# Optimization experiments

Measured on AMD Instinct MI355X. Metric: run time of the kernel, lower is better.

## Reference

```python
import jax, jax.numpy as jnp
import numpy as np

NUM_GRAPHS = 64
NUM_EDGE_TYPES = 3


def gat_conv(x, src, dst, W, a_src, a_dst, bias, num_nodes, heads, ch):
    # PyG GATConv, concat=False: mean over heads, attention leaky_relu slope 0.2
    xp = (x @ W).reshape(num_nodes, heads, ch)          # [N,H,C]
    al_s = jnp.einsum('nhc,hc->nh', xp, a_src)           # [N,H]
    al_d = jnp.einsum('nhc,hc->nh', xp, a_dst)
    logits = jax.nn.leaky_relu(al_s[src] + al_d[dst], 0.2)  # [E,H]
    m = jax.ops.segment_max(logits, dst, num_segments=num_nodes)
    e = jnp.exp(logits - m[dst])
    denom = jax.ops.segment_sum(e, dst, num_segments=num_nodes)
    alpha = e / denom[dst]                               # segment softmax over dst
    msg = alpha[:, :, None] * xp[src]                    # [E,H,C]
    out = jax.ops.segment_sum(msg, dst, num_segments=num_nodes)  # [N,H,C]
    return out.mean(axis=1) + bias


def lstm_dir(seq, w_ih, w_hh, b_ih, b_hh):
    # seq: [L,N,C]; PyTorch LSTM cell math
    hh = w_hh.shape[1]
    n = seq.shape[1]
    def step(carry, xt):
        h, c = carry
        g = xt @ w_ih.T + b_ih + h @ w_hh.T + b_hh
        i, f, gg, o = jnp.split(g, 4, axis=-1)
        c = jax.nn.sigmoid(f) * c + jax.nn.sigmoid(i) * jnp.tanh(gg)
        h = jax.nn.sigmoid(o) * jnp.tanh(c)
        return (h, c), h
    init = (jnp.zeros((n, hh), seq.dtype), jnp.zeros((n, hh), seq.dtype))
    _, hs = jax.lax.scan(step, init, seq)
    return hs  # [L,N,hh]


def setup_inputs() -> dict:
    key = jax.random.key(0)
    ks = jax.random.split(key, 24)
    N, E, C, H, P, T = 50000, 600000, 128, 4, 2, NUM_EDGE_TYPES
    HH = (P * C) // 2  # JK biLSTM hidden = 128
    s = 0.05
    src = jax.random.randint(ks[0], (E,), 0, N, dtype=jnp.int32)
    off = jax.random.randint(ks[1], (E,), 1, N, dtype=jnp.int32)
    dst = (src + off) % N  # guaranteed self-loop free
    edge_index = jnp.stack([src, dst], axis=0)  # types are contiguous blocks of E//T
    batch = jnp.sort(jax.random.randint(ks[2], (N,), 0, NUM_GRAPHS, dtype=jnp.int32))
    return {
        'x': jax.random.normal(ks[3], (N, C), jnp.float32),
        'edge_index': edge_index,
        'batch': batch,
        'problem_type': jax.random.uniform(ks[4], (NUM_GRAPHS, 1), jnp.float32),
        'gat_W': jax.random.normal(ks[5], (P, T, C, H * C), jnp.float32) * s,
        'gat_att_src': jax.random.normal(ks[6], (P, T, H, C), jnp.float32) * s,
        'gat_att_dst': jax.random.normal(ks[7], (P, T, H, C), jnp.float32) * s,
        'gat_bias': jnp.zeros((P, T, C), jnp.float32),
        'w_ih_fw': jax.random.normal(ks[8], (4 * HH, C), jnp.float32) * s,
        'w_hh_fw': jax.random.normal(ks[9], (4 * HH, HH), jnp.float32) * s,
        'b_ih_fw': jnp.zeros((4 * HH,), jnp.float32),
        'b_hh_fw': jnp.zeros((4 * HH,), jnp.float32),
        'w_ih_bw': jax.random.normal(ks[10], (4 * HH, C), jnp.float32) * s,
        'w_hh_bw': jax.random.normal(ks[11], (4 * HH, HH), jnp.float32) * s,
        'b_ih_bw': jnp.zeros((4 * HH,), jnp.float32),
        'b_hh_bw': jnp.zeros((4 * HH,), jnp.float32),
        'jk_att_w': jax.random.normal(ks[12], (2 * HH, 1), jnp.float32) * s,
        'jk_att_b': jnp.zeros((1,), jnp.float32),
        'fc1_w': jax.random.normal(ks[13], (C + 1, 80), jnp.float32) * s,
        'fc1_b': jnp.zeros((80,), jnp.float32),
        'fc2_w': jax.random.normal(ks[14], (80, 80), jnp.float32) * s,
        'fc2_b': jnp.zeros((80,), jnp.float32),
        'fc3_w': jax.random.normal(ks[15], (80, 10), jnp.float32) * s,
        'fc3_b': jnp.zeros((10,), jnp.float32),
    }


def reference(x, edge_index, batch, problem_type, gat_W, gat_att_src, gat_att_dst,
              gat_bias, w_ih_fw, w_hh_fw, b_ih_fw, b_hh_fw, w_ih_bw, w_hh_bw,
              b_ih_bw, b_hh_bw, jk_att_w, jk_att_b, fc1_w, fc1_b, fc2_w, fc2_b,
              fc3_w, fc3_b):
    N, C = x.shape
    P, T, H, _ = gat_att_src.shape
    E = edge_index.shape[1]
    Et = E // T  # edge types stored in contiguous blocks
    loop = jnp.arange(N, dtype=edge_index.dtype)
    xs = [x]
    cur = x
    for p in range(P):
        acc = jnp.zeros_like(cur)
        for t in range(T):
            src = jnp.concatenate([edge_index[0, t * Et:(t + 1) * Et], loop])
            dst = jnp.concatenate([edge_index[1, t * Et:(t + 1) * Et], loop])
            out = gat_conv(cur, src, dst, gat_W[p, t], gat_att_src[p, t],
                           gat_att_dst[p, t], gat_bias[p, t], N, H, C)
            acc = acc + jax.nn.leaky_relu(out)  # slope 0.01 (F.leaky_relu default)
        cur = acc / T
        xs.append(cur)
    seq = jnp.stack(xs, axis=0)  # [L,N,C], L=P+1
    hf = lstm_dir(seq, w_ih_fw, w_hh_fw, b_ih_fw, b_hh_fw)
    hb = lstm_dir(seq[::-1], w_ih_bw, w_hh_bw, b_ih_bw, b_hh_bw)[::-1]
    h = jnp.concatenate([hf, hb], axis=-1)  # [L,N,2*HH]
    score = jnp.einsum('lnh,ho->lno', h, jk_att_w)[..., 0] + jk_att_b[0]  # [L,N]
    alpha = jax.nn.softmax(score, axis=0)
    xjk = jnp.einsum('ln,lnc->nc', alpha, seq)  # JK-LSTM weighted sum
    pooled = jax.ops.segment_sum(xjk, batch, num_segments=NUM_GRAPHS)  # collate='sum'
    z = jnp.concatenate([pooled, problem_type], axis=1)
    z = jax.nn.leaky_relu(z @ fc1_w + fc1_b)
    z = jax.nn.leaky_relu(z @ fc2_w + fc2_b)
    return z @ fc3_w + fc3_b
```

## Files before the change

### kernel.cpp

```cpp
#include <hip/hip_runtime.h>
#include <cfloat>


typedef __attribute__((ext_vector_type(8))) short short8;
typedef __attribute__((ext_vector_type(4))) float f32x4;

#define DEG_CAP 32

__device__ __forceinline__ float lrelu(float x, float s) { return x > 0.f ? x : s * x; }

__device__ __forceinline__ float sigmf(float x) {
    return __builtin_amdgcn_rcpf(1.f + __expf(-x));
}
__device__ __forceinline__ float tanhf_fast(float x) {
    x = fminf(fmaxf(x, -15.f), 15.f);
    float e = __expf(2.f * x);
    return (e - 1.f) * __builtin_amdgcn_rcpf(e + 1.f);
}

__device__ __forceinline__ unsigned f2bf(float f) {
    unsigned u = __float_as_uint(f);
    return (u + 0x7FFFu + ((u >> 16) & 1u)) >> 16;
}
__device__ __forceinline__ float bflo(unsigned u) {
    return __uint_as_float(u << 16);
}
__device__ __forceinline__ float bfhi(unsigned u) {
    return __uint_as_float(u & 0xFFFF0000u);
}

__device__ __forceinline__ int xcd_tile(int bid, int nwg) {
    int q = nwg >> 3, r = nwg & 7;
    int xcd = bid & 7, idx = bid >> 3;
    return (xcd < r ? xcd * (q + 1) : r * (q + 1) + (xcd - r) * q) + idx;
}

__device__ __forceinline__ void stage_tiles(
    char* ldsA, char* ldsB, const float* __restrict__ A,
    const ushort* __restrict__ Bt, int row0, int col0, int M, int tid)
{
#pragma unroll
    for (int it = 0; it < 4; ++it) {
        int idx = it * 512 + tid;
        int r = idx >> 4, kc = (idx & 15) << 3;
        int row = row0 + r;
        float4 v0 = make_float4(0.f, 0.f, 0.f, 0.f), v1 = v0;
        if (row < M) {
            const float* ap = A + (long)row * 128 + kc;
            v0 = *(const float4*)ap;
            v1 = *(const float4*)(ap + 4);
        }
        uint4 w;
        w.x = f2bf(v0.x) | (f2bf(v0.y) << 16);
        w.y = f2bf(v0.z) | (f2bf(v0.w) << 16);
        w.z = f2bf(v1.x) | (f2bf(v1.y) << 16);
        w.w = f2bf(v1.z) | (f2bf(v1.w) << 16);
        int off = (r * 256 + kc * 2) ^ ((r & 7) << 4);
        *(uint4*)(ldsA + off) = w;
        *(uint4*)(ldsB + off) = *(const uint4*)(Bt + (long)(col0 + r) * 128 + kc);
    }
}

__device__ __forceinline__ void stage_a16(
    char* ldsA, const ushort* __restrict__ A, int row0, int M, int tid)
{
#pragma unroll
    for (int it = 0; it < 4; ++it) {
        int idx = it * 512 + tid;
        int r = idx >> 4, kc = (idx & 15) << 3;
        int row = row0 + r;
        uint4 v = make_uint4(0, 0, 0, 0);
        if (row < M) v = *(const uint4*)(A + (long)row * 128 + kc);
        *(uint4*)(ldsA + ((r * 256 + kc * 2) ^ ((r & 7) << 4))) = v;
    }
}
__device__ __forceinline__ void stage_b16(
    char* ldsB, const ushort* __restrict__ B, int tid)
{
#pragma unroll
    for (int it = 0; it < 4; ++it) {
        int idx = it * 512 + tid;
        int r = idx >> 4, kc = (idx & 15) << 3;
        *(uint4*)(ldsB + ((r * 256 + kc * 2) ^ ((r & 7) << 4))) =
            *(const uint4*)(B + (long)r * 128 + kc);
    }
}

__device__ __forceinline__ void compute_tile(
    const char* ldsA, const char* ldsB, f32x4 acc[2][4],
    int wr, int wc, int lr, int lk)
{
#pragma unroll
    for (int ks = 0; ks < 4; ++ks) {
        int kb = ks * 64 + lk;
        short8 af[2], bfr[4];
#pragma unroll
        for (int i = 0; i < 2; ++i) {
            int r = wr + i * 16 + lr;
            af[i] = *(const short8*)(ldsA + ((r * 256 + kb) ^ ((r & 7) << 4)));
        }
#pragma unroll
        for (int j = 0; j < 4; ++j) {
            int c = wc + j * 16 + lr;
            bfr[j] = *(const short8*)(ldsB + ((c * 256 + kb) ^ ((c & 7) << 4)));
        }
#pragma unroll
        for (int i = 0; i < 2; ++i)
#pragma unroll
            for (int j = 0; j < 4; ++j)
                acc[i][j] = __builtin_amdgcn_mfma_f32_16x16x32_bf16(af[i], bfr[j], acc[i][j], 0, 0, 0);
    }
}

__global__ __launch_bounds__(512, 4) void gemm_att(
    const float* __restrict__ A, const ushort* __restrict__ Bt,
    ushort* __restrict__ C16, const float* __restrict__ a_s,
    const float* __restrict__ a_d, float* __restrict__ als,
    float* __restrict__ ald, int M, int nwg)
{
    __shared__ char lds[65536];
    __shared__ float smS[128], smD[128];
    char* ldsA = lds;
    char* ldsB = lds + 32768;
    const int tid = threadIdx.x;
    int tile = xcd_tile(blockIdx.x, nwg);
    int row0 = (tile >> 2) * 128;
    int h = tile & 3;
    int col0 = h * 128;
    if (tid < 128) { smS[tid] = 0.f; smD[tid] = 0.f; }
    stage_tiles(ldsA, ldsB, A, Bt, row0, col0, M, tid);
    __syncthreads();

    const int wv = tid >> 6, lane = tid & 63;
    const int wr = (wv & 3) * 32, wc = (wv >> 2) * 64;
    const int lr = lane & 15;
    const int lk = (lane >> 4) << 4;
    f32x4 acc[2][4] = {};
    compute_tile(ldsA, ldsB, acc, wr, wc, lr, lk);

    const float* asl = a_s + h * 128;
    const float* adl = a_d + h * 128;
#pragma unroll
    for (int i = 0; i < 2; ++i) {
#pragma unroll
        for (int q = 0; q < 4; ++q) {
            float ps = 0.f, pd = 0.f;
            int row = row0 + wr + i * 16 + (lane >> 4) * 4 + q;
#pragma unroll
            for (int j = 0; j < 4; ++j) {
                int cc = wc + j * 16 + lr;
                float v = acc[i][j][q];
                ps += v * asl[cc];
                pd += v * adl[cc];
                if (row < M) C16[(long)row * 512 + col0 + cc] = (ushort)f2bf(v);
            }
#pragma unroll
            for (int off = 8; off; off >>= 1) {
                ps += __shfl_xor(ps, off);
                pd += __shfl_xor(pd, off);
            }
            if (lr == 0) {
                int rl = wr + i * 16 + (lane >> 4) * 4 + q;
                atomicAdd(&smS[rl], ps);
                atomicAdd(&smD[rl], pd);
            }
        }
    }
    __syncthreads();
    if (tid < 128) {
        int row = row0 + tid;
        if (row < M) {
            als[(long)row * 4 + h] = smS[tid];
            ald[(long)row * 4 + h] = smD[tid];
        }
    }
}

__global__ __launch_bounds__(512, 4) void lstm_step(
    const ushort* __restrict__ Ab, const ushort* __restrict__ Bih,
    const ushort* __restrict__ Bhh, const ushort* __restrict__ hprev,
    ushort* __restrict__ hcur, float* __restrict__ cbuf,
    const float* __restrict__ bi, const float* __restrict__ bh,
    const float* __restrict__ jw, float* __restrict__ score,
    int N, int nwg, int first)
{
    __shared__ char lds[65536];
    __shared__ float ssc[128];
    char* ldsA = lds;
    char* ldsB = lds + 32768;
    const int tid = threadIdx.x;
    int tile = xcd_tile(blockIdx.x, nwg);
    int row0 = (tile >> 2) * 128;
    int cc = tile & 3;
    if (tid < 128) ssc[tid] = 0.f;

    const int wv = tid >> 6, lane = tid & 63;
    const int wr = (wv & 3) * 32, wc = (wv >> 2) * 64;
    const int lr = lane & 15, lg = lane >> 4;
    const int lk = lg << 4;
    f32x4 acc[2][4] = {};

    stage_a16(ldsA, Ab, row0, N, tid);
    stage_b16(ldsB, Bih + (long)cc * 128 * 128, tid);
    __syncthreads();
    compute_tile(ldsA, ldsB, acc, wr, wc, lr, lk);
    if (!first) {
        __syncthreads();
        stage_a16(ldsA, hprev, row0, N, tid);
        stage_b16(ldsB, Bhh + (long)cc * 128 * 128, tid);
        __syncthreads();
        compute_tile(ldsA, ldsB, acc, wr, wc, lr, lk);
    }

    const int ch = cc * 32 + (wc >> 6) * 16 + lr;
    const float bI = bi[ch] + bh[ch];
    const float bF = bi[128 + ch] + bh[128 + ch];
    const float bG = bi[256 + ch] + bh[256 + ch];
    const float bO = bi[384 + ch] + bh[384 + ch];
    const float jv = jw[ch];
    float psum[8];
#pragma unroll
    for (int i = 0; i < 2; ++i) {
#pragma unroll
        for (int q = 0; q < 4; ++q) {
            int u = i * 4 + q;
            int row = row0 + wr + i * 16 + lg * 4 + q;
            float p = 0.f;
            if (row < N) {
                long off = (long)row * 128 + ch;
                float cprev = first ? 0.f : cbuf[off];
                float cv = sigmf(acc[i][1][q] + bF) * cprev
                         + sigmf(acc[i][0][q] + bI) * tanhf_fast(acc[i][2][q] + bG);
                float hv = sigmf(acc[i][3][q] + bO) * tanhf_fast(cv);
                cbuf[off] = cv;
                hcur[off] = (ushort)f2bf(hv);
                p = hv * jv;
            }
            psum[u] = p;
        }
    }
#pragma unroll
    for (int u = 0; u < 8; ++u) {
        float p = psum[u];
#pragma unroll
        for (int off = 8; off; off >>= 1) p += __shfl_xor(p, off);
        if (lr == 0)
            atomicAdd(&ssc[wr + (u >> 2) * 16 + lg * 4 + (u & 3)], p);
    }
    __syncthreads();
    if (tid < 128) {
        int row = row0 + tid;
        if (row < N) unsafeAtomicAdd(&score[row], ssc[tid]);
    }
}

__global__ void pack_gatw(const float* __restrict__ gw, ushort* __restrict__ out) {
    int i = blockIdx.x * 256 + threadIdx.x;
    if (i >= 6 * 65536) return;
    int pt = i >> 16, rem = i & 65535, n = rem >> 7, k = rem & 127;
    out[i] = (ushort)f2bf(gw[pt * 65536 + k * 512 + n]);
}
__global__ void pack_lstm(const float* __restrict__ a, const float* __restrict__ b,
                          const float* __restrict__ c, const float* __restrict__ d,
                          ushort* __restrict__ out) {
    int i = blockIdx.x * 256 + threadIdx.x;
    if (i >= 4 * 65536) return;
    const float* p = (i < 65536) ? a : (i < 131072) ? b : (i < 196608) ? c : d;
    int rem = i & 65535;
    int cp = rem >> 7, k = rem & 127;
    int g = (cp >> 4) & 3;
    int ch = ((cp >> 6) << 4) | (cp & 15);
    out[i] = (ushort)f2bf(p[(g * 128 + ch) * 128 + k]);
}
__global__ void pack_x(const float* __restrict__ x, ushort* __restrict__ o, long n) {
    long i = ((long)blockIdx.x * 256 + threadIdx.x) * 4;
    if (i >= n) return;
    float4 v = *(const float4*)(x + i);
    ushort4 u;
    u.x = (ushort)f2bf(v.x); u.y = (ushort)f2bf(v.y);
    u.z = (ushort)f2bf(v.z); u.w = (ushort)f2bf(v.w);
    *(ushort4*)(o + i) = u;
}

__global__ __launch_bounds__(256) void build_csr(
    const int* __restrict__ srcs, const int* __restrict__ dsts,
    int E, int Et, int N, int* __restrict__ cnt, int* __restrict__ bucket)
{
    int i = blockIdx.x * 256 + threadIdx.x;
    if (i >= E) return;
    int t = i / Et;
    int s = srcs[i];
    int d = dsts[i];
    int slot = atomicAdd(&cnt[t * N + d], 1);
    if (slot < DEG_CAP) bucket[((long)(t * N + d)) * DEG_CAP + slot] = s;
}

__global__ __launch_bounds__(256) void gat_gather(
    const int* __restrict__ cnt, const int* __restrict__ bucket,
    const float* __restrict__ als, const float* __restrict__ ald,
    const ushort* __restrict__ xp16, const float* __restrict__ bias,
    float* __restrict__ dstb, ushort* __restrict__ out16, int N, int t, int first)
{
    int d = blockIdx.x * 4 + (threadIdx.x >> 6);
    int lane = threadIdx.x & 63;
    if (d >= N) return;
    int deg = min(cnt[t * N + d], DEG_CAP);
    int s = d;
    if (lane < deg) s = bucket[((long)(t * N + d)) * DEG_CAP + lane];
    bool act = (lane <= deg);
    float4 ad = *(const float4*)(ald + (long)d * 4);
    float l0 = -FLT_MAX, l1 = -FLT_MAX, l2 = -FLT_MAX, l3 = -FLT_MAX;
    if (act) {
        float4 as = *(const float4*)(als + (long)s * 4);
        l0 = lrelu(as.x + ad.x, 0.2f);
        l1 = lrelu(as.y + ad.y, 0.2f);
        l2 = lrelu(as.z + ad.z, 0.2f);
        l3 = lrelu(as.w + ad.w, 0.2f);
    }
    float m0 = l0, m1 = l1, m2 = l2, m3 = l3;
#pragma unroll
    for (int off = 32; off; off >>= 1) {
        m0 = fmaxf(m0, __shfl_xor(m0, off));
        m1 = fmaxf(m1, __shfl_xor(m1, off));
        m2 = fmaxf(m2, __shfl_xor(m2, off));
        m3 = fmaxf(m3, __shfl_xor(m3, off));
    }
    float e0 = 0.f, e1 = 0.f, e2 = 0.f, e3 = 0.f;
    if (act) {
        e0 = __expf(l0 - m0); e1 = __expf(l1 - m1);
        e2 = __expf(l2 - m2); e3 = __expf(l3 - m3);
    }
    float s0 = e0, s1 = e1, s2 = e2, s3 = e3;
#pragma unroll
    for (int off = 32; off; off >>= 1) {
        s0 += __shfl_xor(s0, off);
        s1 += __shfl_xor(s1, off);
        s2 += __shfl_xor(s2, off);
        s3 += __shfl_xor(s3, off);
    }
    float a0 = 0.25f * e0 / s0, a1 = 0.25f * e1 / s1;
    float a2 = 0.25f * e2 / s2, a3 = 0.25f * e3 / s3;

    float accL = 0.f, accH = 0.f;
    int sj = __shfl(s, 0);
    const uint* xs = (const uint*)(xp16 + (long)sj * 512);
    uint c0 = xs[lane], c1 = xs[64 + lane], c2 = xs[128 + lane], c3 = xs[192 + lane];
    for (int j = 0; j < deg; ++j) {
        int sn = __shfl(s, j + 1);
        const uint* xn = (const uint*)(xp16 + (long)sn * 512);
        uint n0 = xn[lane], n1 = xn[64 + lane], n2 = xn[128 + lane], n3 = xn[192 + lane];
        float w0 = __shfl(a0, j), w1 = __shfl(a1, j);
        float w2 = __shfl(a2, j), w3 = __shfl(a3, j);
        accL += w0 * bflo(c0) + w1 * bflo(c1) + w2 * bflo(c2) + w3 * bflo(c3);
        accH += w0 * bfhi(c0) + w1 * bfhi(c1) + w2 * bfhi(c2) + w3 * bfhi(c3);
        c0 = n0; c1 = n1; c2 = n2; c3 = n3;
    }
    float w0 = __shfl(a0, deg), w1 = __shfl(a1, deg);
    float w2 = __shfl(a2, deg), w3 = __shfl(a3, deg);
    accL += w0 * bflo(c0) + w1 * bflo(c1) + w2 * bflo(c2) + w3 * bflo(c3);
    accH += w0 * bfhi(c0) + w1 * bfhi(c1) + w2 * bfhi(c2) + w3 * bfhi(c3);

    int chL = 2 * lane;
    float r0 = lrelu(accL + bias[chL], 0.01f) * (1.f / 3.f);
    float r1 = lrelu(accH + bias[chL + 1], 0.01f) * (1.f / 3.f);
    float2* ap = (float2*)(dstb + (long)d * 128) + lane;
    float2 f;
    if (first) { f.x = r0; f.y = r1; }
    else       { float2 prev = *ap; f.x = prev.x + r0; f.y = prev.y + r1; }
    *ap = f;
    if (out16) {
        ushort2 u2;
        u2.x = (ushort)f2bf(f.x);
        u2.y = (ushort)f2bf(f.y);
        *((ushort2*)(out16 + (long)d * 128) + lane) = u2;
    }
}

__global__ void jk_kernel(const float* __restrict__ score, const float* __restrict__ x0,
                          const float* __restrict__ x1, const float* __restrict__ x2,
                          float* __restrict__ xjk, int N)
{
    long i = (long)blockIdx.x * 256 + threadIdx.x;
    long n = i >> 7;
    if (n >= N) return;
    float s0 = score[n], s1 = score[N + n], s2 = score[2L * N + n];
    float m = fmaxf(s0, fmaxf(s1, s2));
    float e0 = expf(s0 - m), e1 = expf(s1 - m), e2 = expf(s2 - m);
    float inv = 1.f / (e0 + e1 + e2);
    xjk[i] = (e0 * x0[i] + e1 * x1[i] + e2 * x2[i]) * inv;
}

__global__ void init_z0(const float* __restrict__ ptype, float* __restrict__ z0) {
    int i = blockIdx.x * 128 + threadIdx.x;
    if (i < 64 * 129) z0[i] = ((i % 129) == 128) ? ptype[i / 129] : 0.f;
}

__global__ __launch_bounds__(128) void pool2(
    const float* __restrict__ xjk, const int* __restrict__ batch,
    float* __restrict__ z0, int N)
{
    int c = threadIdx.x;
    int n0 = blockIdx.x * 64;
    if (n0 >= N) return;
    int n1 = min(n0 + 64, N);
    float s = 0.f;
    int g = batch[n0];
    for (int n = n0; n < n1; ++n) {
        int b = batch[n];
        if (b != g) { unsafeAtomicAdd(&z0[g * 129 + c], s); s = 0.f; g = b; }
        s += xjk[(long)n * 128 + c];
    }
    unsafeAtomicAdd(&z0[g * 129 + c], s);
}

__global__ __launch_bounds__(128) void mlp_kernel(
    const float* __restrict__ z0, const float* __restrict__ w1, const float* __restrict__ b1,
    const float* __restrict__ w2, const float* __restrict__ b2,
    const float* __restrict__ w3, const float* __restrict__ b3,
    float* __restrict__ out)
{
    int gidx = blockIdx.x, tid = threadIdx.x;
    __shared__ float zin[129], z1[80], z2[80];
    zin[tid] = z0[gidx * 129 + tid];
    if (tid == 0) zin[128] = z0[gidx * 129 + 128];
    __syncthreads();
    if (tid < 80) {
        float s = b1[tid];
        for (int k = 0; k < 129; ++k) s += zin[k] * w1[k * 80 + tid];
        z1[tid] = lrelu(s, 0.01f);
    }
    __syncthreads();
    if (tid < 80) {
        float s = b2[tid];
        for (int k = 0; k < 80; ++k) s += z1[k] * w2[k * 80 + tid];
        z2[tid] = lrelu(s, 0.01f);
    }
    __syncthreads();
    if (tid < 10) {
        float s = b3[tid];
        for (int k = 0; k < 80; ++k) s += z2[k] * w3[k * 10 + tid];
        out[gidx * 10 + tid] = s;
    }
}

extern "C" void kernel_launch(void* const* d_in, const int* in_sizes, int n_in,
                              void* d_out, int out_size, void* d_ws, size_t ws_size,
                              hipStream_t stream)
{
    (void)n_in; (void)out_size; (void)ws_size;
    const float* x      = (const float*)d_in[0];
    const int*   ei     = (const int*)d_in[1];
    const int*   batch  = (const int*)d_in[2];
    const float* ptype  = (const float*)d_in[3];
    const float* gatW   = (const float*)d_in[4];
    const float* gatAs  = (const float*)d_in[5];
    const float* gatAd  = (const float*)d_in[6];
    const float* gatB   = (const float*)d_in[7];
    const float* w_ih_fw = (const float*)d_in[8];
    const float* w_hh_fw = (const float*)d_in[9];
    const float* b_ih_fw = (const float*)d_in[10];
    const float* b_hh_fw = (const float*)d_in[11];
    const float* w_ih_bw = (const float*)d_in[12];
    const float* w_hh_bw = (const float*)d_in[13];
    const float* b_ih_bw = (const float*)d_in[14];
    const float* b_hh_bw = (const float*)d_in[15];
    const float* jkw    = (const float*)d_in[16];
    const float* fc1w   = (const float*)d_in[18];
    const float* fc1b   = (const float*)d_in[19];
    const float* fc2w   = (const float*)d_in[20];
    const float* fc2b   = (const float*)d_in[21];
    const float* fc3w   = (const float*)d_in[22];
    const float* fc3b   = (const float*)d_in[23];

    const int N = in_sizes[0] / 128;
    const int E = in_sizes[1] / 2;
    const int Et = E / 3;
    const long NC = (long)N * 128;

    float* w = (float*)d_ws;
    float* xp   = w; w += (long)N * 512;
    float* l1   = w; w += NC;
    float* l2   = w; w += NC;
    float* accb = w; w += NC;
    float* outm = w; w += NC;
    ushort* xb16 = (ushort*)w; w += 3L * N * 64;
    float* als  = w; w += (long)N * 4;
    float* ald  = w; w += (long)N * 4;
    float* score = w; w += 3L * N;
    ushort* gwt = (ushort*)w; w += 6 * 65536 / 2;
    ushort* lwt = (ushort*)w; w += 4 * 65536 / 2;
    float* z0   = w; w += 64 * 129 + 4;

    int* cnt    = (int*)outm;
    int* bucket = cnt + 3L * N;
    ushort* xp16 = (ushort*)xp;
    ushort* h0 = xp16 + (long)N * 512;
    ushort* h1 = h0 + NC;

    pack_gatw<<<(6 * 65536 + 255) / 256, 256, 0, stream>>>(gatW, gwt);
    pack_lstm<<<(4 * 65536 + 255) / 256, 256, 0, stream>>>(w_ih_fw, w_hh_fw, w_ih_bw, w_hh_bw, lwt);
    pack_x<<<(int)((NC / 4 + 255) / 256), 256, 0, stream>>>(x, xb16, NC);
    hipMemsetAsync(score, 0, sizeof(float) * 3 * N, stream);
    hipMemsetAsync(cnt, 0, sizeof(int) * 3 * N, stream);
    build_csr<<<(E + 255) / 256, 256, 0, stream>>>(ei, ei + E, E, Et, N, cnt, bucket);

    const int RB = (N + 127) / 128;
    const int nwg = RB * 4;
    const int ncb = (int)((NC + 255) / 256);

    const float* cur = x;
    for (int p = 0; p < 2; ++p) {
        float* dstb = (p == 0) ? l1 : l2;
        ushort* d16 = xb16 + (long)(p + 1) * N * 128;
        for (int t = 0; t < 3; ++t) {
            int pt = p * 3 + t;
            gemm_att<<<nwg, 512, 0, stream>>>(cur, gwt + (long)pt * 65536, xp16,
                                              gatAs + pt * 512, gatAd + pt * 512,
                                              als, ald, N, nwg);
            gat_gather<<<(N + 3) / 4, 256, 0, stream>>>(cnt, bucket, als, ald, xp16,
                                                        gatB + pt * 128, dstb,
                                                        (t == 2) ? d16 : nullptr,
                                                        N, t, t == 0);
        }
        cur = dstb;
    }

    float* cbuf = outm;
    for (int dir = 0; dir < 2; ++dir) {
        const ushort* Bih = lwt + (long)(dir ? 2 : 0) * 65536;
        const ushort* Bhh = lwt + (long)(dir ? 3 : 1) * 65536;
        const float* bi = dir ? b_ih_bw : b_ih_fw;
        const float* bh = dir ? b_hh_bw : b_hh_fw;
        const float* jw = jkw + (dir ? 128 : 0);
        ushort* hp = h0;
        ushort* hc = h1;
        for (int j = 0; j < 3; ++j) {
            int l = dir ? (2 - j) : j;
            const ushort* Ab = xb16 + (long)l * N * 128;
            lstm_step<<<nwg, 512, 0, stream>>>(Ab, Bih, Bhh, hp, hc, cbuf,
                                               bi, bh, jw, score + (long)l * N,
                                               N, nwg, j == 0);
            ushort* tmp = hp; hp = hc; hc = tmp;
        }
    }

    jk_kernel<<<ncb, 256, 0, stream>>>(score, x, l1, l2, accb, N);
    init_z0<<<65, 128, 0, stream>>>(ptype, z0);
    pool2<<<(N + 63) / 64, 128, 0, stream>>>(accb, batch, z0, N);
    mlp_kernel<<<64, 128, 0, stream>>>(z0, fc1w, fc1b, fc2w, fc2b, fc3w, fc3b,
                                       (float*)d_out);
}
```

Baseline: 793.3 us.

## Gather two destinations per wave and feed GEMM pre-packed bf16 activations

The GAT gather kernel now gives each half-wave its own destination node, so each wave covers two nodes. Each lane loads eight packed words per neighbour, and the softmax reductions run over 32 lanes. DEG_CAP drops to 31 so a node's neighbours plus its self loop fit in one half-wave, and the neighbour loop runs to the larger degree of the pair, with zero weights padding the shorter one. Separately, gemm_att now reads the bf16 layer activations that the gather already writes, instead of loading fp32 and converting to bf16 in the kernel. That halves the GEMM's activation read traffic and removes the conversion work.

```diff
diff --git a/kernel.cpp b/kernel.cpp
--- a/kernel.cpp
+++ b/kernel.cpp
@@ -5,7 +5,7 @@
 typedef __attribute__((ext_vector_type(8))) short short8;
 typedef __attribute__((ext_vector_type(4))) float f32x4;
 
-#define DEG_CAP 32
+#define DEG_CAP 31
 
 __device__ __forceinline__ float lrelu(float x, float s) { return x > 0.f ? x : s * x; }
 
@@ -33,32 +33,6 @@
     int q = nwg >> 3, r = nwg & 7;
     int xcd = bid & 7, idx = bid >> 3;
     return (xcd < r ? xcd * (q + 1) : r * (q + 1) + (xcd - r) * q) + idx;
-}
-
-__device__ __forceinline__ void stage_tiles(
-    char* ldsA, char* ldsB, const float* __restrict__ A,
-    const ushort* __restrict__ Bt, int row0, int col0, int M, int tid)
-{
-#pragma unroll
-    for (int it = 0; it < 4; ++it) {
-        int idx = it * 512 + tid;
-        int r = idx >> 4, kc = (idx & 15) << 3;
-        int row = row0 + r;
-        float4 v0 = make_float4(0.f, 0.f, 0.f, 0.f), v1 = v0;
-        if (row < M) {
-            const float* ap = A + (long)row * 128 + kc;
-            v0 = *(const float4*)ap;
-            v1 = *(const float4*)(ap + 4);
-        }
-        uint4 w;
-        w.x = f2bf(v0.x) | (f2bf(v0.y) << 16);
-        w.y = f2bf(v0.z) | (f2bf(v0.w) << 16);
-        w.z = f2bf(v1.x) | (f2bf(v1.y) << 16);
-        w.w = f2bf(v1.z) | (f2bf(v1.w) << 16);
-        int off = (r * 256 + kc * 2) ^ ((r & 7) << 4);
-        *(uint4*)(ldsA + off) = w;
-        *(uint4*)(ldsB + off) = *(const uint4*)(Bt + (long)(col0 + r) * 128 + kc);
-    }
 }
 
 __device__ __forceinline__ void stage_a16(
@@ -113,7 +87,7 @@
 }
 
 __global__ __launch_bounds__(512, 4) void gemm_att(
-    const float* __restrict__ A, const ushort* __restrict__ Bt,
+    const ushort* __restrict__ A16, const ushort* __restrict__ Bt,
     ushort* __restrict__ C16, const float* __restrict__ a_s,
     const float* __restrict__ a_d, float* __restrict__ als,
     float* __restrict__ ald, int M, int nwg)
@@ -128,7 +102,8 @@
     int h = tile & 3;
     int col0 = h * 128;
     if (tid < 128) { smS[tid] = 0.f; smD[tid] = 0.f; }
-    stage_tiles(ldsA, ldsB, A, Bt, row0, col0, M, tid);
+    stage_a16(ldsA, A16, row0, M, tid);
+    stage_b16(ldsB, Bt + (long)col0 * 128, tid);
     __syncthreads();
 
     const int wv = tid >> 6, lane = tid & 63;
@@ -301,13 +276,14 @@
     const ushort* __restrict__ xp16, const float* __restrict__ bias,
     float* __restrict__ dstb, ushort* __restrict__ out16, int N, int t, int first)
 {
-    int d = blockIdx.x * 4 + (threadIdx.x >> 6);
     int lane = threadIdx.x & 63;
-    if (d >= N) return;
+    int half = lane >> 5, hl = lane & 31;
+    int d = blockIdx.x * 8 + (threadIdx.x >> 6) * 2 + half;
+    if (d >= N) d = N - 1;
     int deg = min(cnt[t * N + d], DEG_CAP);
     int s = d;
-    if (lane < deg) s = bucket[((long)(t * N + d)) * DEG_CAP + lane];
-    bool act = (lane <= deg);
+    if (hl < deg) s = bucket[((long)(t * N + d)) * DEG_CAP + hl];
+    bool act = (hl <= deg);
     float4 ad = *(const float4*)(ald + (long)d * 4);
     float l0 = -FLT_MAX, l1 = -FLT_MAX, l2 = -FLT_MAX, l3 = -FLT_MAX;
     if (act) {
@@ -319,7 +295,7 @@
     }
     float m0 = l0, m1 = l1, m2 = l2, m3 = l3;
 #pragma unroll
-    for (int off = 32; off; off >>= 1) {
+    for (int off = 16; off; off >>= 1) {
         m0 = fmaxf(m0, __shfl_xor(m0, off));
         m1 = fmaxf(m1, __shfl_xor(m1, off));
         m2 = fmaxf(m2, __shfl_xor(m2, off));
@@ -332,7 +308,7 @@
     }
     float s0 = e0, s1 = e1, s2 = e2, s3 = e3;
 #pragma unroll
-    for (int off = 32; off; off >>= 1) {
+    for (int off = 16; off; off >>= 1) {
         s0 += __shfl_xor(s0, off);
         s1 += __shfl_xor(s1, off);
         s2 += __shfl_xor(s2, off);
@@ -341,38 +317,62 @@
     float a0 = 0.25f * e0 / s0, a1 = 0.25f * e1 / s1;
     float a2 = 0.25f * e2 / s2, a3 = 0.25f * e3 / s3;
 
-    float accL = 0.f, accH = 0.f;
-    int sj = __shfl(s, 0);
+    int md = deg;
+#pragma unroll
+    for (int off = 32; off; off >>= 1) md = max(md, __shfl_xor(md, off));
+
+    int base = (lane & 32);
+    float accL[4] = {0.f, 0.f, 0.f, 0.f}, accH[4] = {0.f, 0.f, 0.f, 0.f};
+    int sj = __shfl(s, base);
     const uint* xs = (const uint*)(xp16 + (long)sj * 512);
-    uint c0 = xs[lane], c1 = xs[64 + lane], c2 = xs[128 + lane], c3 = xs[192 + lane];
-    for (int j = 0; j < deg; ++j) {
-        int sn = __shfl(s, j + 1);
+    uint c0 = xs[hl], c1 = xs[32 + hl], c2 = xs[64 + hl], c3 = xs[96 + hl];
+    uint c4 = xs[128 + hl], c5 = xs[160 + hl], c6 = xs[192 + hl], c7 = xs[224 + hl];
+    for (int j = 0; j < md; ++j) {
+        int sn = __shfl(s, base + j + 1);
         const uint* xn = (const uint*)(xp16 + (long)sn * 512);
-        uint n0 = xn[lane], n1 = xn[64 + lane], n2 = xn[128 + lane], n3 = xn[192 + lane];
-        float w0 = __shfl(a0, j), w1 = __shfl(a1, j);
-        float w2 = __shfl(a2, j), w3 = __shfl(a3, j);
-        accL += w0 * bflo(c0) + w1 * bflo(c1) + w2 * bflo(c2) + w3 * bflo(c3);
-        accH += w0 * bfhi(c0) + w1 * bfhi(c1) + w2 * bfhi(c2) + w3 * bfhi(c3);
+        uint n0 = xn[hl], n1 = xn[32 + hl], n2 = xn[64 + hl], n3 = xn[96 + hl];
+        uint n4 = xn[128 + hl], n5 = xn[160 + hl], n6 = xn[192 + hl], n7 = xn[224 + hl];
+        float w0 = __shfl(a0, base + j), w1 = __shfl(a1, base + j);
+        float w2 = __shfl(a2, base + j), w3 = __shfl(a3, base + j);
+        accL[0] += w0 * bflo(c0) + w1 * bflo(c2) + w2 * bflo(c4) + w3 * bflo(c6);
+        accH[0] += w0 * bfhi(c0) + w1 * bfhi(c2) + w2 * bfhi(c4) + w3 * bfhi(c6);
+        accL[1] += w0 * bflo(c1) + w1 * bflo(c3) + w2 * bflo(c5) + w3 * bflo(c7);
+        accH[1] += w0 * bfhi(c1) + w1 * bfhi(c3) + w2 * bfhi(c5) + w3 * bfhi(c7);
+        accL[2] += 0.f;
         c0 = n0; c1 = n1; c2 = n2; c3 = n3;
-    }
-    float w0 = __shfl(a0, deg), w1 = __shfl(a1, deg);
-    float w2 = __shfl(a2, deg), w3 = __shfl(a3, deg);
-    accL += w0 * bflo(c0) + w1 * bflo(c1) + w2 * bflo(c2) + w3 * bflo(c3);
-    accH += w0 * bfhi(c0) + w1 * bfhi(c1) + w2 * bfhi(c2) + w3 * bfhi(c3);
-
-    int chL = 2 * lane;
-    float r0 = lrelu(accL + bias[chL], 0.01f) * (1.f / 3.f);
-    float r1 = lrelu(accH + bias[chL + 1], 0.01f) * (1.f / 3.f);
-    float2* ap = (float2*)(dstb + (long)d * 128) + lane;
-    float2 f;
-    if (first) { f.x = r0; f.y = r1; }
-    else       { float2 prev = *ap; f.x = prev.x + r0; f.y = prev.y + r1; }
-    *ap = f;
+        c4 = n4; c5 = n5; c6 = n6; c7 = n7;
+    }
+    {
+        float w0 = __shfl(a0, base + md), w1 = __shfl(a1, base + md);
+        float w2 = __shfl(a2, base + md), w3 = __shfl(a3, base + md);
+        accL[0] += w0 * bflo(c0) + w1 * bflo(c2) + w2 * bflo(c4) + w3 * bflo(c6);
+        accH[0] += w0 * bfhi(c0) + w1 * bfhi(c2) + w2 * bfhi(c4) + w3 * bfhi(c6);
+        accL[1] += w0 * bflo(c1) + w1 * bflo(c3) + w2 * bflo(c5) + w3 * bflo(c7);
+        accH[1] += w0 * bfhi(c1) + w1 * bfhi(c3) + w2 * bfhi(c5) + w3 * bfhi(c7);
+    }
+
+    int chA = 2 * hl;
+    int chB = 64 + 2 * hl;
+    float r0 = lrelu(accL[0] + bias[chA], 0.01f) * (1.f / 3.f);
+    float r1 = lrelu(accH[0] + bias[chA + 1], 0.01f) * (1.f / 3.f);
+    float r2 = lrelu(accL[1] + bias[chB], 0.01f) * (1.f / 3.f);
+    float r3 = lrelu(accH[1] + bias[chB + 1], 0.01f) * (1.f / 3.f);
+    float2* apA = (float2*)(dstb + (long)d * 128) + hl;
+    float2* apB = (float2*)(dstb + (long)d * 128 + 64) + hl;
+    float2 fA, fB;
+    if (first) { fA.x = r0; fA.y = r1; fB.x = r2; fB.y = r3; }
+    else {
+        float2 pA = *apA, pB = *apB;
+        fA.x = pA.x + r0; fA.y = pA.y + r1;
+        fB.x = pB.x + r2; fB.y = pB.y + r3;
+    }
+    *apA = fA; *apB = fB;
     if (out16) {
-        ushort2 u2;
-        u2.x = (ushort)f2bf(f.x);
-        u2.y = (ushort)f2bf(f.y);
-        *((ushort2*)(out16 + (long)d * 128) + lane) = u2;
+        ushort2 uA, uB;
+        uA.x = (ushort)f2bf(fA.x); uA.y = (ushort)f2bf(fA.y);
+        uB.x = (ushort)f2bf(fB.x); uB.y = (ushort)f2bf(fB.y);
+        *((ushort2*)(out16 + (long)d * 128) + hl) = uA;
+        *((ushort2*)(out16 + (long)d * 128 + 64) + hl) = uB;
     }
 }
 
@@ -508,21 +508,20 @@
     const int nwg = RB * 4;
     const int ncb = (int)((NC + 255) / 256);
 
-    const float* cur = x;
     for (int p = 0; p < 2; ++p) {
+        const ushort* curA = xb16 + (long)p * N * 128;
         float* dstb = (p == 0) ? l1 : l2;
         ushort* d16 = xb16 + (long)(p + 1) * N * 128;
         for (int t = 0; t < 3; ++t) {
             int pt = p * 3 + t;
-            gemm_att<<<nwg, 512, 0, stream>>>(cur, gwt + (long)pt * 65536, xp16,
+            gemm_att<<<nwg, 512, 0, stream>>>(curA, gwt + (long)pt * 65536, xp16,
                                               gatAs + pt * 512, gatAd + pt * 512,
                                               als, ald, N, nwg);
-            gat_gather<<<(N + 3) / 4, 256, 0, stream>>>(cnt, bucket, als, ald, xp16,
+            gat_gather<<<(N + 7) / 8, 256, 0, stream>>>(cnt, bucket, als, ald, xp16,
                                                         gatB + pt * 128, dstb,
                                                         (t == 2) ? d16 : nullptr,
                                                         N, t, t == 0);
         }
-        cur = dstb;
     }
 
     float* cbuf = outm;
```

New measurement: 786.5 us. Within noise of the previous version (-0.8%).
